# Kernel optimization log

Hardware: AMD Instinct MI355X
Metric: run time of the kernel (lower is better)

The kernel has to match this reference:

```python
import jax, jax.numpy as jnp
import numpy as np

D_MODEL = 1024
N_HEADS = 16
HEAD_DIM = D_MODEL // N_HEADS
NEG_INF = -1e30


def _rotary(v):
    # v: [B, H, T, hd]. Original module rotates each (even, odd) pair by 90 deg:
    # out[..., 2i] = -v[..., 2i+1]; out[..., 2i+1] = v[..., 2i]
    v2 = v.reshape(*v.shape[:-1], HEAD_DIM // 2, 2)
    return jnp.stack([-v2[..., 1], v2[..., 0]], axis=-1).reshape(v.shape)


def setup_inputs() -> dict:
    key = jax.random.key(0)
    ks = jax.random.split(key, 9)
    B, T, D = 2, 2048, D_MODEL
    s = 1.0 / np.sqrt(D)
    inp = {
        "x": jax.random.normal(ks[0], (B, T, D), dtype=jnp.float32),
        "Wq_w": jax.random.normal(ks[1], (D, D), dtype=jnp.float32) * s,
        "Wq_b": jnp.zeros((D,), dtype=jnp.float32),
        "Wk_w": jax.random.normal(ks[2], (D, D), dtype=jnp.float32) * s,
        "Wk_b": jnp.zeros((D,), dtype=jnp.float32),
        "Wv_w": jax.random.normal(ks[3], (D, D), dtype=jnp.float32) * s,
        "Wv_b": jnp.zeros((D,), dtype=jnp.float32),
        "Wo_w": jax.random.normal(ks[4], (D, D), dtype=jnp.float32) * s,
        "Wo_b": jnp.zeros((D,), dtype=jnp.float32),
    }
    # create_sparse_mask: block-diagonal True windows of size T//4
    window = T // 4
    blk = jnp.arange(T) // window
    inp["sparse_mask"] = blk[:, None] == blk[None, :]
    return inp


def reference(x, Wq_w, Wq_b, Wk_w, Wk_b, Wv_w, Wv_b, Wo_w, Wo_b, sparse_mask):
    B, T, D = x.shape
    H, hd = N_HEADS, HEAD_DIM

    def proj(w, b):  # [B,T,D] -> [B,H,T,hd]
        return (x @ w.T + b).reshape(B, T, H, hd).transpose(0, 2, 1, 3)

    q = _rotary(proj(Wq_w, Wq_b))
    k = _rotary(proj(Wk_w, Wk_b))
    v = proj(Wv_w, Wv_b)

    scores = jnp.einsum("bhqd,bhkd->bhqk", q, k) / jnp.sqrt(jnp.asarray(hd, x.dtype))
    causal = jnp.tril(jnp.ones((T, T), dtype=bool))
    allowed = sparse_mask & causal  # block-diagonal AND causal
    scores = jnp.where(allowed, scores, NEG_INF)
    attn = jax.nn.softmax(scores, axis=-1)  # dropout_p=0.1 omitted (eval mode)
    out = jnp.einsum("bhqk,bhkd->bhqd", attn, v)
    out = out.transpose(0, 2, 1, 3).reshape(B, T, D)
    return out @ Wo_w.T + Wo_b
```

## Files before the change

### kernel.cpp

```cpp
#include <hip/hip_runtime.h>
#include <hip/hip_bf16.h>
#include <stdint.h>

typedef __attribute__((ext_vector_type(4))) float f32x4;
typedef __attribute__((ext_vector_type(8))) __bf16 bf16x8;
typedef __attribute__((ext_vector_type(4))) unsigned short u16x4;
typedef __attribute__((ext_vector_type(8))) unsigned short u16x8;
typedef __attribute__((ext_vector_type(2))) unsigned int u32x2;
typedef const __attribute__((address_space(1))) void* as1_cvp;
typedef __attribute__((address_space(3))) void* as3_vp;

#define LOG2E 1.44269504088896340736f

#define VMW0() asm volatile("s_waitcnt vmcnt(0)" ::: "memory")
#define VMW2() asm volatile("s_waitcnt vmcnt(2)" ::: "memory")
#define VMW4() asm volatile("s_waitcnt vmcnt(4)" ::: "memory")
#define VMW6() asm volatile("s_waitcnt vmcnt(6)" ::: "memory")
#define BAR()  do { __builtin_amdgcn_sched_barrier(0); __builtin_amdgcn_s_barrier(); \
                    __builtin_amdgcn_sched_barrier(0); } while (0)

static __device__ __forceinline__ unsigned short f2bf(float f) {
  union { float f; unsigned int u; } c; c.f = f;
  unsigned int r = c.u + 0x7FFFu + ((c.u >> 16) & 1u);
  return (unsigned short)(r >> 16);
}

static __device__ __forceinline__ void gl_lds16(const void* g, void* l) {
  __builtin_amdgcn_global_load_lds((as1_cvp)(uintptr_t)g, (as3_vp)(uintptr_t)l, 16, 0, 0);
}

__global__ __launch_bounds__(256) void cvt_kernel(
    const float* __restrict__ x, const float* __restrict__ wq, const float* __restrict__ wk,
    const float* __restrict__ wv, const float* __restrict__ wo,
    unsigned short* __restrict__ xb, unsigned short* __restrict__ wqb,
    unsigned short* __restrict__ wkb, unsigned short* __restrict__ wvb,
    unsigned short* __restrict__ wob) {
  long e = ((long)blockIdx.x * 256 + threadIdx.x) * 8;
  const float* s; unsigned short* d; long o;
  if (e < 4194304)      { s = x;  d = xb;  o = e; }
  else if (e < 5242880) { s = wq; d = wqb; o = e - 4194304; }
  else if (e < 6291456) { s = wk; d = wkb; o = e - 5242880; }
  else if (e < 7340032) { s = wv; d = wvb; o = e - 6291456; }
  else                  { s = wo; d = wob; o = e - 7340032; }
  float4 a = *(const float4*)(s + o);
  float4 b = *(const float4*)(s + o + 4);
  u16x8 v;
  v[0] = f2bf(a.x); v[1] = f2bf(a.y); v[2] = f2bf(a.z); v[3] = f2bf(a.w);
  v[4] = f2bf(b.x); v[5] = f2bf(b.y); v[6] = f2bf(b.z); v[7] = f2bf(b.w);
  *(u16x8*)(d + o) = v;
}

__global__ __launch_bounds__(512, 4) void gemm_qkv8(
    const unsigned short* __restrict__ xb, const unsigned short* __restrict__ wcat,
    const float* __restrict__ bq, const float* __restrict__ bk, const float* __restrict__ bv,
    unsigned short* __restrict__ qo, unsigned short* __restrict__ ko,
    unsigned short* __restrict__ vto) {
  __shared__ __align__(16) char lds[81920];
  const int tid = threadIdx.x;
  const int lane = tid & 63, wid = tid >> 6;
  const int wm = wid >> 2, wn = wid & 3;
  const int c = lane & 15, g = lane >> 4;

  const int bid = blockIdx.x;
  const int xcd = bid & 7, idx = bid >> 3;
  const int m0 = (((xcd >> 1) << 3) + idx / 12) << 7;
  const int n0 = (((xcd & 1) * 12) + idx % 12) << 7;

  const int sj = tid >> 3;
  const int sg = (tid & 7) ^ (sj & 7);
  const long soff = (((long)(sj + ((sg >> 2) << 6))) << 11) + ((sg & 3) << 4);
  const char* Ab = (const char*)xb;
  const char* Bb = (const char*)wcat;

  const int sA = ((((wm << 2) | g) ^ (c & 7)) << 4);
  const int sB = (((((wn >> 1) << 2) | g) ^ (c & 7)) << 4);
  const char* pAr = lds + (c << 7) + sA;
  const char* pBr = lds + 8192 + ((((wn & 1) << 5) + c) << 7) + sB;

  f32x4 acc[4][2] = {};

  auto STAGE = [&](int t, int slot) {
    char* db = lds + slot * 16384;
    const long ko = (long)t << 6;
    gl_lds16(Ab + ((long)m0 << 11) + soff + ko, db + tid * 16);
    gl_lds16(Bb + ((long)n0 << 11) + soff + ko, db + 8192 + tid * 16);
  };

  STAGE(0, 0); STAGE(1, 1); STAGE(2, 2); STAGE(3, 3);

  int rs = 0, ss = 4;
#pragma unroll 1
  for (int t = 0; t < 32; ++t) {
    if (t <= 28) { VMW6(); }
    else if (t == 29) { VMW4(); }
    else if (t == 30) { VMW2(); }
    else { VMW0(); }
    BAR();

    const int sb = rs * 16384;
    bf16x8 aa[4];
#pragma unroll
    for (int f = 0; f < 4; ++f) aa[f] = *(const bf16x8*)(pAr + sb + (f << 11));
    bf16x8 bb0 = *(const bf16x8*)(pBr + sb);
    bf16x8 bb1 = *(const bf16x8*)(pBr + sb + 2048);
    __builtin_amdgcn_s_setprio(1);
#pragma unroll
    for (int f = 0; f < 4; ++f)
      acc[f][0] = __builtin_amdgcn_mfma_f32_16x16x32_bf16(aa[f], bb0, acc[f][0], 0, 0, 0);
#pragma unroll
    for (int f = 0; f < 4; ++f)
      acc[f][1] = __builtin_amdgcn_mfma_f32_16x16x32_bf16(aa[f], bb1, acc[f][1], 0, 0, 0);
    __builtin_amdgcn_s_setprio(0);

    if (t + 4 < 32) STAGE(t + 4, ss);

    rs = (rs == 4) ? 0 : rs + 1;
    ss = (ss == 4) ? 0 : ss + 1;
  }

#pragma unroll
  for (int nf = 0; nf < 2; ++nf) {
    const int n = n0 + (wn << 5) + (nf << 4) + c;
    const int z = n >> 10, nn = n & 1023;
    const float bb_ = (z == 0 ? bq : z == 1 ? bk : bv)[nn];
    const float sc = (z == 0) ? 0.125f : 1.0f;
    const int h = nn >> 6, dd = nn & 63;
#pragma unroll
    for (int f = 0; f < 4; ++f) {
      const int mb = m0 + (wm << 6) + (f << 4) + (g << 2);
      const int b = mb >> 11, tt = mb & 2047;
      if (z < 2) {
        unsigned short* dst = (z == 0 ? qo : ko) +
            ((((long)(b << 4) + h) << 11) + tt) * 64 + dd;
#pragma unroll
        for (int j = 0; j < 4; ++j) dst[(long)j * 64] = f2bf((acc[f][nf][j] + bb_) * sc);
      } else {
        u16x4 pk;
#pragma unroll
        for (int j = 0; j < 4; ++j) pk[j] = f2bf(acc[f][nf][j] + bb_);
        *(u16x4*)(vto + ((((long)((b << 4) + h) << 6) + dd) << 11) + tt) = pk;
      }
    }
  }
}

__global__ __launch_bounds__(512, 4) void gemm_oproj8(
    const unsigned short* __restrict__ ab, const unsigned short* __restrict__ wob,
    const float* __restrict__ bo, float* __restrict__ out) {
  __shared__ __align__(16) char lds[49152];
  const int tid = threadIdx.x;
  const int lane = tid & 63, wid = tid >> 6;
  const int wm = wid >> 2, wn = wid & 3;
  const int c = lane & 15, g = lane >> 4;

  const int bid = blockIdx.x;
  const int xcd = bid & 7, idx = bid >> 3;
  const int m0 = ((xcd << 3) + (idx >> 3)) << 6;
  const int n0 = (idx & 7) << 7;

  const int srow = tid >> 3;
  const int coff = (((tid & 7) ^ (srow & 7)) << 4);
  const char* Ab = (const char*)ab;
  const char* Bb = (const char*)wob;

  const int swzr0 = ((g ^ (c & 7)) << 4);
  const int swzr1 = (((4 | g) ^ (c & 7)) << 4);

  f32x4 acc[2][2] = {};

  auto STAGE = [&](int kt, int unit) {
    char* db = lds + (kt & 1) * 24576;
    const char* gp; char* dst;
    if (unit == 0) {
      gp = Ab + ((long)(m0 + srow) << 11) + (kt << 7) + coff;
      dst = db + tid * 16;
    } else {
      gp = Bb + ((long)(n0 + (unit - 1) * 64 + srow) << 11) + (kt << 7) + coff;
      dst = db + unit * 8192 + tid * 16;
    }
    gl_lds16(gp, dst);
  };

  STAGE(0, 0); STAGE(0, 1); STAGE(0, 2);
  VMW0();
  BAR();

#pragma unroll 1
  for (int kt = 0; kt < 16; ++kt) {
    const int bufb = (kt & 1) * 24576;
    if (kt < 15) { STAGE(kt + 1, 0); STAGE(kt + 1, 1); STAGE(kt + 1, 2); }
    bf16x8 aa[2][2];
    const char* pA = lds + bufb + (wm << 12) + (c << 7);
#pragma unroll
    for (int f = 0; f < 2; ++f) {
      aa[f][0] = *(const bf16x8*)(pA + (f << 11) + swzr0);
      aa[f][1] = *(const bf16x8*)(pA + (f << 11) + swzr1);
    }
#pragma unroll
    for (int nf = 0; nf < 2; ++nf) {
      const int rB = (wn << 5) + (nf << 4) + c;
      const char* pB = lds + bufb + 8192 + ((rB >> 6) << 13) + ((rB & 63) << 7);
      bf16x8 b0 = *(const bf16x8*)(pB + swzr0);
      bf16x8 b1 = *(const bf16x8*)(pB + swzr1);
      __builtin_amdgcn_s_setprio(1);
#pragma unroll
      for (int f = 0; f < 2; ++f)
        acc[f][nf] = __builtin_amdgcn_mfma_f32_16x16x32_bf16(aa[f][0], b0, acc[f][nf], 0, 0, 0);
#pragma unroll
      for (int f = 0; f < 2; ++f)
        acc[f][nf] = __builtin_amdgcn_mfma_f32_16x16x32_bf16(aa[f][1], b1, acc[f][nf], 0, 0, 0);
      __builtin_amdgcn_s_setprio(0);
    }
    if (kt < 15) VMW0();
    BAR();
  }

#pragma unroll
  for (int nf = 0; nf < 2; ++nf) {
    const int n = n0 + (wn << 5) + (nf << 4) + c;
    const float bb = bo[n];
#pragma unroll
    for (int f = 0; f < 2; ++f) {
      const int mb = m0 + (wm << 5) + (f << 4) + (g << 2);
#pragma unroll
      for (int j = 0; j < 4; ++j)
        out[((long)(mb + j) << 10) + n] = acc[f][nf][j] + bb;
    }
  }
}

__global__ __launch_bounds__(512) void attn_kernel(
    const unsigned short* __restrict__ qg, const unsigned short* __restrict__ kg,
    const unsigned short* __restrict__ vtg, unsigned short* __restrict__ og) {
  __shared__ __align__(16) char kv_s[3][16384];
  __shared__ __align__(16) char p_s[8][2304];

  const int bx = blockIdx.x, bh = blockIdx.y;
  const int map1[16] = {3,7,11,15, 2,6,10,14, 0,4,8,12, 1,5,9,13};
  const int map2[16] = {0,4,8,12, 1,5,9,13, 3,7,11,15, 2,6,10,14};
  const int qt = (bh < 16) ? map1[bx] : map2[bx];
  const int tid = threadIdx.x;
  const int lane = tid & 63, w = tid >> 6;
  const int c = lane & 15, g = lane >> 4;
  const int q0 = qt << 7;
  const int wstart = q0 & ~511;
  const int nt = ((q0 - wstart) >> 6) + 2;

  const unsigned short* qrow = qg + (((long)bh << 11) + q0 + (w << 4) + c) * 64;
  bf16x8 qa0 = *(const bf16x8*)(qrow + (g << 3));
  bf16x8 qa1 = *(const bf16x8*)(qrow + (g << 3) + 32);

  float m_run = -3.0e38f, l_run = 0.0f;
  f32x4 oacc[4] = {};

  const int sr = tid >> 3;
  const int jx16 = (((tid & 7) ^ (sr & 7)) << 4);
  const char* kbase = (const char*)kg + ((((long)bh << 11) + sr) << 7) + jx16;
  const char* vbase = (const char*)vtg + ((((long)bh << 6) + sr) << 12) + jx16;
  const int t16 = tid << 4;

  auto STAGEKV = [&](int kv0, int bsel) {
    char* dst = kv_s[bsel];
    gl_lds16(kbase + ((long)kv0 << 7), dst + t16);
    gl_lds16(vbase + ((long)kv0 << 1), dst + 8192 + t16);
  };

  STAGEKV(wstart, 0);
  STAGEKV(wstart + 64, 1);

  int rsel = 0, ssel = 2;
  for (int t = 0; t < nt; ++t) {
    if (t + 1 < nt) VMW2(); else VMW0();
    BAR();

    const char* kb_ = kv_s[rsel];
    const char* vb_ = kv_s[rsel] + 8192;
    const int kv0 = wstart + (t << 6);

    f32x4 sacc[4] = {};
    __builtin_amdgcn_s_setprio(1);
#pragma unroll
    for (int mf = 0; mf < 4; ++mf) {
      const int kr = (mf << 4) + c;
      const char* kp = kb_ + (kr << 7);
      bf16x8 k0 = *(const bf16x8*)(kp + ((g ^ (kr & 7)) << 4));
      bf16x8 k1 = *(const bf16x8*)(kp + (((4 | g) ^ (kr & 7)) << 4));
      sacc[mf] = __builtin_amdgcn_mfma_f32_16x16x32_bf16(k0, qa0, sacc[mf], 0, 0, 0);
      sacc[mf] = __builtin_amdgcn_mfma_f32_16x16x32_bf16(k1, qa1, sacc[mf], 0, 0, 0);
    }
    __builtin_amdgcn_s_setprio(0);

    const int dkv = kv0 - q0;
    if (dkv > (w << 4) - 64) {
      const int qrel = (w << 4) + c;
#pragma unroll
      for (int mf = 0; mf < 4; ++mf)
#pragma unroll
        for (int j = 0; j < 4; ++j)
          if (dkv + (mf << 4) + (g << 2) + j > qrel) sacc[mf][j] = -3.0e38f;
    }

    float pm[4];
#pragma unroll
    for (int mf = 0; mf < 4; ++mf)
      pm[mf] = fmaxf(fmaxf(sacc[mf][0], sacc[mf][1]), fmaxf(sacc[mf][2], sacc[mf][3]));
    float pmax = fmaxf(fmaxf(pm[0], pm[1]), fmaxf(pm[2], pm[3]));
    pmax = fmaxf(pmax, __shfl_xor(pmax, 16));
    pmax = fmaxf(pmax, __shfl_xor(pmax, 32));

    const bool resc = !__all(pmax <= m_run + 8.0f);
    const float m_new = resc ? fmaxf(m_run, pmax) : m_run;

    const float mL = m_new * LOG2E;
    float ls[4];
#pragma unroll
    for (int mf = 0; mf < 4; ++mf) {
      float p0 = __builtin_amdgcn_exp2f(__builtin_fmaf(sacc[mf][0], LOG2E, -mL));
      float p1 = __builtin_amdgcn_exp2f(__builtin_fmaf(sacc[mf][1], LOG2E, -mL));
      float p2 = __builtin_amdgcn_exp2f(__builtin_fmaf(sacc[mf][2], LOG2E, -mL));
      float p3 = __builtin_amdgcn_exp2f(__builtin_fmaf(sacc[mf][3], LOG2E, -mL));
      sacc[mf][0] = p0; sacc[mf][1] = p1; sacc[mf][2] = p2; sacc[mf][3] = p3;
      ls[mf] = (p0 + p1) + (p2 + p3);
    }
    float lsum = (ls[0] + ls[1]) + (ls[2] + ls[3]);
    lsum += __shfl_xor(lsum, 16);
    lsum += __shfl_xor(lsum, 32);

    if (resc) {
      const float alpha = __builtin_amdgcn_exp2f((m_run - m_new) * LOG2E);
      l_run *= alpha;
#pragma unroll
      for (int j = 0; j < 4; ++j) {
        const float aj = __shfl(alpha, (g << 2) + j);
#pragma unroll
        for (int nf = 0; nf < 4; ++nf) oacc[nf][j] *= aj;
      }
      m_run = m_new;
    }
    l_run += lsum;

    {
      char* pw = p_s[w] + c * 144;
#pragma unroll
      for (int mf = 0; mf < 4; ++mf) {
        unsigned int p01, p23;
        asm("v_cvt_pk_bf16_f32 %0, %1, %2" : "=v"(p01) : "v"(sacc[mf][0]), "v"(sacc[mf][1]));
        asm("v_cvt_pk_bf16_f32 %0, %1, %2" : "=v"(p23) : "v"(sacc[mf][2]), "v"(sacc[mf][3]));
        u32x2 pk; pk[0] = p01; pk[1] = p23;
        *(u32x2*)(pw + (mf << 5) + (g << 3)) = pk;
      }
    }

    const char* pr = p_s[w] + c * 144;
    __builtin_amdgcn_s_setprio(1);
#pragma unroll
    for (int kk = 0; kk < 2; ++kk) {
      bf16x8 pa = *(const bf16x8*)(pr + (kk << 6) + (g << 4));
#pragma unroll
      for (int nf = 0; nf < 4; ++nf) {
        const int vr = (nf << 4) + c;
        bf16x8 vb = *(const bf16x8*)(vb_ + (vr << 7) +
                                     ((((kk << 2) | g) ^ (vr & 7)) << 4));
        oacc[nf] = __builtin_amdgcn_mfma_f32_16x16x32_bf16(pa, vb, oacc[nf], 0, 0, 0);
      }
    }
    __builtin_amdgcn_s_setprio(0);

    if (t + 2 < nt) STAGEKV(wstart + ((t + 2) << 6), ssel);

    rsel = (rsel == 2) ? 0 : rsel + 1;
    ssel = (ssel == 2) ? 0 : ssel + 1;
  }

  const int b = bh >> 4, h = bh & 15;
#pragma unroll
  for (int j = 0; j < 4; ++j) {
    const float linv = 1.0f / __shfl(l_run, (g << 2) + j);
    const int trow = q0 + (w << 4) + (g << 2) + j;
    unsigned short* dst = og + ((((long)(b << 11)) + trow) << 10) + (h << 6);
#pragma unroll
    for (int nf = 0; nf < 4; ++nf)
      dst[(nf << 4) + c] = f2bf(oacc[nf][j] * linv);
  }
}

extern "C" void kernel_launch(void* const* d_in, const int* in_sizes, int n_in,
                              void* d_out, int out_size, void* d_ws, size_t ws_size,
                              hipStream_t stream) {
  const float* x  = (const float*)d_in[0];
  const float* wq = (const float*)d_in[1];
  const float* bq = (const float*)d_in[2];
  const float* wk = (const float*)d_in[3];
  const float* bk = (const float*)d_in[4];
  const float* wv = (const float*)d_in[5];
  const float* bv = (const float*)d_in[6];
  const float* wo = (const float*)d_in[7];
  const float* bo = (const float*)d_in[8];

  char* ws = (char*)d_ws;
  unsigned short* xb    = (unsigned short*)(ws);
  unsigned short* wqb   = (unsigned short*)(ws + 8388608);
  unsigned short* wkb   = (unsigned short*)(ws + 10485760);
  unsigned short* wvb   = (unsigned short*)(ws + 12582912);
  unsigned short* wob   = (unsigned short*)(ws + 14680064);
  unsigned short* qb    = (unsigned short*)(ws + 16777216);
  unsigned short* kb    = (unsigned short*)(ws + 25165824);
  unsigned short* vtb   = (unsigned short*)(ws + 33554432);
  unsigned short* attnb = xb;

  cvt_kernel<<<4096, 256, 0, stream>>>(x, wq, wk, wv, wo, xb, wqb, wkb, wvb, wob);
  gemm_qkv8<<<768, 512, 0, stream>>>(xb, wqb, bq, bk, bv, qb, kb, vtb);
  attn_kernel<<<dim3(16, 32), 512, 0, stream>>>(qb, kb, vtb, attnb);
  gemm_oproj8<<<512, 512, 0, stream>>>(attnb, wob, bo, (float*)d_out);
}
```

Baseline: 77.44 us.

## Switch GEMM and attention to double-buffered LDS pipelines for higher occupancy

Replaces the 5-stage LDS ring in the QKV GEMM and the 3-stage K/V ring in attention with 2-slot double buffering. The next tile is prefetched right after the barrier and waited on fully each iteration. This shrinks LDS per block (80KB to 32KB in the GEMM, 48KB to 32KB plus P scratch in attention) and raises launch-bounds occupancy hints so more blocks can be resident. It also remaps the GEMM block-to-tile swizzle across XCDs. The trade-off is a shallower prefetch depth with a full vmcnt(0) stall every iteration, which relies on extra occupancy to hide latency.

```diff
diff --git a/kernel.cpp b/kernel.cpp
--- a/kernel.cpp
+++ b/kernel.cpp
@@ -13,9 +13,6 @@
 #define LOG2E 1.44269504088896340736f
 
 #define VMW0() asm volatile("s_waitcnt vmcnt(0)" ::: "memory")
-#define VMW2() asm volatile("s_waitcnt vmcnt(2)" ::: "memory")
-#define VMW4() asm volatile("s_waitcnt vmcnt(4)" ::: "memory")
-#define VMW6() asm volatile("s_waitcnt vmcnt(6)" ::: "memory")
 #define BAR()  do { __builtin_amdgcn_sched_barrier(0); __builtin_amdgcn_s_barrier(); \
                     __builtin_amdgcn_sched_barrier(0); } while (0)
 
@@ -50,12 +47,12 @@
   *(u16x8*)(d + o) = v;
 }
 
-__global__ __launch_bounds__(512, 4) void gemm_qkv8(
+__global__ __launch_bounds__(512, 6) void gemm_qkv8(
     const unsigned short* __restrict__ xb, const unsigned short* __restrict__ wcat,
     const float* __restrict__ bq, const float* __restrict__ bk, const float* __restrict__ bv,
     unsigned short* __restrict__ qo, unsigned short* __restrict__ ko,
     unsigned short* __restrict__ vto) {
-  __shared__ __align__(16) char lds[81920];
+  __shared__ __align__(16) char lds[32768];
   const int tid = threadIdx.x;
   const int lane = tid & 63, wid = tid >> 6;
   const int wm = wid >> 2, wn = wid & 3;
@@ -63,8 +60,8 @@
 
   const int bid = blockIdx.x;
   const int xcd = bid & 7, idx = bid >> 3;
-  const int m0 = (((xcd >> 1) << 3) + idx / 12) << 7;
-  const int n0 = (((xcd & 1) * 12) + idx % 12) << 7;
+  const int m0 = (((xcd & 1) << 4) + idx / 6) << 7;
+  const int n0 = (((xcd >> 1) * 6) + idx % 6) << 7;
 
   const int sj = tid >> 3;
   const int sg = (tid & 7) ^ (sj & 7);
@@ -86,18 +83,15 @@
     gl_lds16(Bb + ((long)n0 << 11) + soff + ko, db + 8192 + tid * 16);
   };
 
-  STAGE(0, 0); STAGE(1, 1); STAGE(2, 2); STAGE(3, 3);
-
-  int rs = 0, ss = 4;
+  STAGE(0, 0);
+
 #pragma unroll 1
   for (int t = 0; t < 32; ++t) {
-    if (t <= 28) { VMW6(); }
-    else if (t == 29) { VMW4(); }
-    else if (t == 30) { VMW2(); }
-    else { VMW0(); }
+    VMW0();
     BAR();
-
-    const int sb = rs * 16384;
+    if (t + 1 < 32) STAGE(t + 1, (t + 1) & 1);
+
+    const int sb = (t & 1) * 16384;
     bf16x8 aa[4];
 #pragma unroll
     for (int f = 0; f < 4; ++f) aa[f] = *(const bf16x8*)(pAr + sb + (f << 11));
@@ -111,11 +105,6 @@
     for (int f = 0; f < 4; ++f)
       acc[f][1] = __builtin_amdgcn_mfma_f32_16x16x32_bf16(aa[f], bb1, acc[f][1], 0, 0, 0);
     __builtin_amdgcn_s_setprio(0);
-
-    if (t + 4 < 32) STAGE(t + 4, ss);
-
-    rs = (rs == 4) ? 0 : rs + 1;
-    ss = (ss == 4) ? 0 : ss + 1;
   }
 
 #pragma unroll
@@ -229,10 +218,10 @@
   }
 }
 
-__global__ __launch_bounds__(512) void attn_kernel(
+__global__ __launch_bounds__(512, 6) void attn_kernel(
     const unsigned short* __restrict__ qg, const unsigned short* __restrict__ kg,
     const unsigned short* __restrict__ vtg, unsigned short* __restrict__ og) {
-  __shared__ __align__(16) char kv_s[3][16384];
+  __shared__ __align__(16) char kv_s[2][16384];
   __shared__ __align__(16) char p_s[8][2304];
 
   const int bx = blockIdx.x, bh = blockIdx.y;
@@ -266,15 +255,14 @@
   };
 
   STAGEKV(wstart, 0);
-  STAGEKV(wstart + 64, 1);
-
-  int rsel = 0, ssel = 2;
+
   for (int t = 0; t < nt; ++t) {
-    if (t + 1 < nt) VMW2(); else VMW0();
+    VMW0();
     BAR();
-
-    const char* kb_ = kv_s[rsel];
-    const char* vb_ = kv_s[rsel] + 8192;
+    if (t + 1 < nt) STAGEKV(wstart + ((t + 1) << 6), (t + 1) & 1);
+
+    const char* kb_ = kv_s[t & 1];
+    const char* vb_ = kv_s[t & 1] + 8192;
     const int kv0 = wstart + (t << 6);
 
     f32x4 sacc[4] = {};
@@ -365,11 +353,6 @@
       }
     }
     __builtin_amdgcn_s_setprio(0);
-
-    if (t + 2 < nt) STAGEKV(wstart + ((t + 2) << 6), ssel);
-
-    rsel = (rsel == 2) ? 0 : rsel + 1;
-    ssel = (ssel == 2) ? 0 : ssel + 1;
   }
 
   const int b = bh >> 4, h = bh & 15;
```

Measured after the change: 79.59 us. 1.03x slower.
